# Optimization experiments

Measured on AMD Instinct MI355X. Metric: run time of the kernel, lower is better.

## Reference

```python
import jax, jax.numpy as jnp
import numpy as np

B, S, DIM, H = 2, 2048, 1024, 16
HD = DIM // H  # 64


def setup_inputs() -> dict:
    key = jax.random.key(0)
    ks = jax.random.split(key, 7)
    sc = 1.0 / np.sqrt(DIM)
    gammas = jnp.asarray(1.0 - 2.0 ** (-5.0 - np.arange(H)), jnp.float32)  # RetNet per-head decay
    return {
        "q": jax.random.normal(ks[0], (B, S, DIM), jnp.float32),
        "k": jax.random.normal(ks[1], (B, S, DIM), jnp.float32),
        "v": jax.random.normal(ks[2], (B, S, DIM), jnp.float32),
        "W_in": jax.random.normal(ks[3], (DIM, DIM), jnp.float32) * sc,
        "b_in": jnp.zeros((DIM,), jnp.float32),
        "W_gate": jax.random.normal(ks[4], (DIM, DIM), jnp.float32) * sc,
        "b_gate": jnp.zeros((DIM,), jnp.float32),
        "W_out": jax.random.normal(ks[5], (DIM, DIM), jnp.float32) * sc,
        "b_out": jnp.zeros((DIM,), jnp.float32),
        "gammas": gammas,
    }


def _mamba(x, W_in, b_in, W_gate, b_gate, W_out, b_out):
    # Gated linear recurrence: h_t = a_t * h_{t-1} + u_t  (selective-scan style)
    u = x @ W_in + b_in          # [B,S,D]
    a = jax.nn.sigmoid(x @ W_gate + b_gate)  # [B,S,D] data-dependent decay gate

    def combine(c1, c2):
        a1, u1 = c1
        a2, u2 = c2
        return (a1 * a2, a2 * u1 + u2)

    _, h = jax.lax.associative_scan(combine, (a, u), axis=1)  # parallel scan over S
    return h @ W_out + b_out  # residual=False, dropout=0.0


def _retention(q, k, v, gammas):
    # Per-head decay-masked attention: out = ((Q K^T / sqrt(hd)) * D) V,
    # D[h,n,m] = gamma_h^(n-m) for n>=m else 0 (causal decay kernel).
    def split(x):
        return x.reshape(B, S, H, HD).transpose(0, 2, 1, 3)  # [B,H,S,HD]

    qh, kh, vh = split(q), split(k), split(v)
    idx = jnp.arange(S)
    diff = idx[:, None] - idx[None, :]                        # [S,S]
    expnt = jnp.maximum(diff, 0).astype(jnp.float32)
    D = jnp.where(diff >= 0, gammas[:, None, None] ** expnt, 0.0)  # [H,S,S]
    scores = jnp.einsum("bhnd,bhmd->bhnm", qh, kh) / np.sqrt(HD)
    out = jnp.einsum("bhnm,bhmd->bhnd", scores * D[None], vh)
    return out.transpose(0, 2, 1, 3).reshape(B, S, DIM)


def reference(q, k, v, W_in, b_in, W_gate, b_gate, W_out, b_out, gammas):
    q_proj = _mamba(q, W_in, b_in, W_gate, b_gate, W_out, b_out)
    return _retention(q_proj, k, v, gammas)
```

## Files before the change

kernel.cpp:

```cpp
#include <hip/hip_runtime.h>
#include <math.h>

#define B_  2
#define S_  2048
#define D_  1024
#define H_  16
#define HD_ 64
#define M_  (B_*S_)

typedef unsigned short ushort_t;
typedef unsigned int   uint_t;
typedef __attribute__((ext_vector_type(8))) short bf16x8;
typedef __attribute__((ext_vector_type(4))) float f32x4;

__device__ __forceinline__ ushort_t f2bf(float f) {
    uint_t u = __builtin_bit_cast(uint_t, f);
    u += 0x7FFFu + ((u >> 16) & 1u);
    return (ushort_t)(u >> 16);
}
__device__ __forceinline__ float bf2f(ushort_t h) {
    uint_t u = (uint_t)h << 16;
    return __builtin_bit_cast(float, u);
}
__device__ __forceinline__ uint_t pkt(float lo, float hi) {
    return __builtin_amdgcn_perm(__builtin_bit_cast(uint_t, hi),
                                 __builtin_bit_cast(uint_t, lo), 0x07060302u);
}
__device__ __forceinline__ void dma16(const ushort_t* g, ushort_t* l) {
    __builtin_amdgcn_global_load_lds(
        (const __attribute__((address_space(1))) uint_t*)g,
        (__attribute__((address_space(3))) uint_t*)l, 16, 0, 0);
}
__device__ __forceinline__ bf16x8 fragr(const ushort_t* base, int row, int chunk) {
    return *(const bf16x8*)&base[row * 64 + (((chunk ^ (row & 7)) << 3))];
}

__global__ __launch_bounds__(256)
void transp_cvt3(const float* __restrict__ W0, const float* __restrict__ W1,
                 const float* __restrict__ W2, ushort_t* __restrict__ T0,
                 ushort_t* __restrict__ T1, ushort_t* __restrict__ T2) {
    __shared__ float T[32][36];
    const float*  W  = (blockIdx.z == 0) ? W0 : (blockIdx.z == 1) ? W1 : W2;
    ushort_t*     WT = (blockIdx.z == 0) ? T0 : (blockIdx.z == 1) ? T1 : T2;
    const int kt = blockIdx.x, nt = blockIdx.y;
    const int t = threadIdx.x;
    const int rr = t >> 3, cc = (t & 7) * 4;
    float4 w4 = *(const float4*)(W + (size_t)(kt * 32 + rr) * D_ + nt * 32 + cc);
    T[rr][cc + 0] = w4.x; T[rr][cc + 1] = w4.y; T[rr][cc + 2] = w4.z; T[rr][cc + 3] = w4.w;
    __syncthreads();
    ushort_t o[4];
    #pragma unroll
    for (int j = 0; j < 4; ++j) o[j] = f2bf(T[cc + j][rr]);
    *(ushort4*)(WT + (size_t)(nt * 32 + rr) * D_ + kt * 32 + cc) =
        make_ushort4(o[0], o[1], o[2], o[3]);
}

__global__ __launch_bounds__(256)
void cvt_bf16(const float* __restrict__ X, ushort_t* __restrict__ Y) {
    const int i = (blockIdx.x * 256 + threadIdx.x) * 4;
    float4 x = *(const float4*)(X + i);
    *(ushort4*)(Y + i) = make_ushort4(f2bf(x.x), f2bf(x.y), f2bf(x.z), f2bf(x.w));
}

__global__ __launch_bounds__(256)
void kv_cvt_g(const float* __restrict__ K, const float* __restrict__ V,
              const float* __restrict__ gammas, ushort_t* __restrict__ Kb,
              ushort_t* __restrict__ VT, float* __restrict__ Gg) {
    __shared__ ushort_t Tv[64 * 72];
    __shared__ ushort_t Tk[64 * 72];
    const int mt = blockIdx.x, h = blockIdx.y, b = blockIdx.z;
    const int m0 = mt * 64;
    const int tid = threadIdx.x;
    const int r = tid >> 2, c0 = (tid & 3) * 16;
    const float lg = log2f(gammas[h]);
    const float gm = exp2f(-(float)r * lg);
    {
        const float* src = K + ((size_t)(b * S_ + m0 + r)) * D_ + h * HD_ + c0;
        ushort_t kb[16];
        #pragma unroll
        for (int j4 = 0; j4 < 4; ++j4) {
            float4 x = *(const float4*)(src + j4 * 4);
            kb[j4 * 4 + 0] = f2bf(x.x); kb[j4 * 4 + 1] = f2bf(x.y);
            kb[j4 * 4 + 2] = f2bf(x.z); kb[j4 * 4 + 3] = f2bf(x.w);
        }
        ushort_t* dst = Kb + ((size_t)(b * S_ + m0 + r)) * D_ + h * HD_ + c0;
        *(uint4*)(dst + 0) = *(const uint4*)&kb[0];
        *(uint4*)(dst + 8) = *(const uint4*)&kb[8];
        #pragma unroll
        for (int j = 0; j < 16; ++j) Tk[(c0 + j) * 72 + r] = kb[j];
    }
    {
        const float* src = V + ((size_t)(b * S_ + m0 + r)) * D_ + h * HD_ + c0;
        #pragma unroll
        for (int j4 = 0; j4 < 4; ++j4) {
            float4 x = *(const float4*)(src + j4 * 4);
            Tv[(c0 + j4 * 4 + 0) * 72 + r] = f2bf(x.x * gm);
            Tv[(c0 + j4 * 4 + 1) * 72 + r] = f2bf(x.y * gm);
            Tv[(c0 + j4 * 4 + 2) * 72 + r] = f2bf(x.z * gm);
            Tv[(c0 + j4 * 4 + 3) * 72 + r] = f2bf(x.w * gm);
        }
    }
    __syncthreads();
    {
        ushort_t* dst = VT + ((size_t)((b * H_ + h) * HD_ + r)) * S_ + m0 + c0;
        *(uint4*)(dst + 0) = *(const uint4*)&Tv[r * 72 + c0 + 0];
        *(uint4*)(dst + 8) = *(const uint4*)&Tv[r * 72 + c0 + 8];
    }
    const int w = tid >> 6, lane = tid & 63, quad = lane >> 4, l15 = lane & 15;
    bf16x8 af0 = *(const bf16x8*)&Tv[(w * 16 + l15) * 72 + quad * 8];
    bf16x8 af1 = *(const bf16x8*)&Tv[(w * 16 + l15) * 72 + 32 + quad * 8];
    float* gout = Gg + ((size_t)((b * H_ + h) * 32 + mt)) * 4096;
    #pragma unroll
    for (int kt2 = 0; kt2 < 4; ++kt2) {
        bf16x8 bf0 = *(const bf16x8*)&Tk[(kt2 * 16 + l15) * 72 + quad * 8];
        bf16x8 bf1 = *(const bf16x8*)&Tk[(kt2 * 16 + l15) * 72 + 32 + quad * 8];
        f32x4 g = {};
        g = __builtin_amdgcn_mfma_f32_16x16x32_bf16(af0, bf0, g, 0, 0, 0);
        g = __builtin_amdgcn_mfma_f32_16x16x32_bf16(af1, bf1, g, 0, 0, 0);
        #pragma unroll
        for (int reg = 0; reg < 4; ++reg)
            gout[(w * 16 + quad * 4 + reg) * 64 + kt2 * 16 + l15] = g[reg];
    }
}

__global__ __launch_bounds__(256)
void gemm_dual_scan(const ushort_t* __restrict__ A, const ushort_t* __restrict__ BTi,
                    const ushort_t* __restrict__ BTg, const float* __restrict__ bi,
                    const float* __restrict__ bg, float* __restrict__ Hloc,
                    ushort_t* __restrict__ Pp, float* __restrict__ cA,
                    float* __restrict__ cU) {
    __shared__ ushort_t smem[32768];
    const int tid = threadIdx.x;
    const int n0 = blockIdx.x * 64, m0 = blockIdx.y * 128;
    const int w = tid >> 6, lane = tid & 63, quad = lane >> 4, l15 = lane & 15;
    const int wr = (w >> 1) * 64, wc = (w & 1) * 32;
    const int l8 = lane & 7, lr8 = lane >> 3;

    f32x4 acc_i[4][2] = {};
    f32x4 acc_g[4][2] = {};

    auto stage = [&](int k0, int bufo) {
        #pragma unroll
        for (int t = 0; t < 4; ++t) {
            const int row = w * 32 + t * 8 + lr8;
            const int gc = ((l8 ^ (row & 7)) << 3);
            dma16(A + (size_t)(m0 + row) * D_ + k0 + gc, &smem[bufo + row * 64 + l8 * 8]);
        }
        #pragma unroll
        for (int t = 0; t < 2; ++t) {
            const int row = w * 16 + t * 8 + lr8;
            const int gc = ((l8 ^ (row & 7)) << 3);
            dma16(BTi + (size_t)(n0 + row) * D_ + k0 + gc, &smem[bufo + 8192 + row * 64 + l8 * 8]);
            dma16(BTg + (size_t)(n0 + row) * D_ + k0 + gc, &smem[bufo + 12288 + row * 64 + l8 * 8]);
        }
    };

    stage(0, 0);
    __syncthreads();
    for (int t = 0; t < 16; ++t) {
        const int bufo = (t & 1) * 16384;
        if (t < 15) stage((t + 1) * 64, 16384 - bufo);
        const ushort_t* As = smem + bufo;
        const ushort_t* Bi = smem + bufo + 8192;
        const ushort_t* Bg = smem + bufo + 12288;
        #pragma unroll
        for (int kk = 0; kk < 2; ++kk) {
            bf16x8 af[4], bfi[2], bfg[2];
            #pragma unroll
            for (int i = 0; i < 4; ++i)
                af[i] = fragr(As, wr + 16 * i + l15, kk * 4 + quad);
            #pragma unroll
            for (int j = 0; j < 2; ++j) {
                bfi[j] = fragr(Bi, wc + 16 * j + l15, kk * 4 + quad);
                bfg[j] = fragr(Bg, wc + 16 * j + l15, kk * 4 + quad);
            }
            #pragma unroll
            for (int i = 0; i < 4; ++i)
                #pragma unroll
                for (int j = 0; j < 2; ++j) {
                    acc_i[i][j] = __builtin_amdgcn_mfma_f32_16x16x32_bf16(
                        af[i], bfi[j], acc_i[i][j], 0, 0, 0);
                    acc_g[i][j] = __builtin_amdgcn_mfma_f32_16x16x32_bf16(
                        af[i], bfg[j], acc_g[i][j], 0, 0, 0);
                }
        }
        __syncthreads();
    }

    ushort_t* Us = smem;
    ushort_t* Gu = smem + 8448;
    #pragma unroll
    for (int j = 0; j < 2; ++j) {
        const int n = wc + 16 * j + l15;
        const float bbi = bi[n0 + n], bbg = bg[n0 + n];
        #pragma unroll
        for (int i = 0; i < 4; ++i) {
            #pragma unroll
            for (int r = 0; r < 4; ++r) {
                const int m = wr + 16 * i + quad * 4 + r;
                Us[m * 66 + n] = f2bf(acc_i[i][j][r] + bbi);
                float g = 1.0f / (1.0f + __expf(-(acc_g[i][j][r] + bbg)));
                Gu[m * 66 + n] = (ushort_t)__float2uint_rn(g * 65535.0f);
            }
        }
    }
    __syncthreads();

    const int nl = tid & 63, c = tid >> 6;
    const int gmb = m0 + c * 32;
    const size_t gbase = (size_t)gmb * D_ + n0 + nl;
    float Aa = 1.0f, hh = 0.0f;
    #pragma unroll 4
    for (int j = 0; j < 32; ++j) {
        const float g = (float)Gu[(c * 32 + j) * 66 + nl] * (1.0f / 65535.0f);
        const float u = bf2f(Us[(c * 32 + j) * 66 + nl]);
        Aa *= g;
        hh = fmaf(g, hh, u);
        Pp[gbase + (size_t)j * D_] = f2bf(Aa);
        Hloc[gbase + (size_t)j * D_] = hh;
    }
    const int bb = gmb >> 11;
    const int ch = (gmb & 2047) >> 5;
    const int ci = ((bb * 64 + ch) << 10) + n0 + nl;
    cA[ci] = Aa;
    cU[ci] = hh;
}

__global__ __launch_bounds__(256)
void mid_scan(const float* __restrict__ Gg, const float* __restrict__ gammas,
              ushort_t* __restrict__ Sb, const float* __restrict__ cA,
              const float* __restrict__ cU, float* __restrict__ cIn) {
    const int bi = blockIdx.x;
    if (bi < 128) {
        const int sl = bi & 3, h = (bi >> 2) & 15, b = bi >> 6;
        const float g64 = exp2f(64.0f * log2f(gammas[h]));
        const int r = threadIdx.x >> 4;
        const int cb = (threadIdx.x & 15) * 4;
        const size_t base = ((size_t)((b * H_ + h) * 32)) * 4096 + (sl * 16 + r) * 64 + cb;
        float4 S = make_float4(0.f, 0.f, 0.f, 0.f);
        for (int c = 0; c < 32; ++c) {
            ushort4 sb;
            sb.x = f2bf(S.x); sb.y = f2bf(S.y); sb.z = f2bf(S.z); sb.w = f2bf(S.w);
            *(ushort4*)(Sb + base + (size_t)c * 4096) = sb;
            float4 G = *(const float4*)(Gg + base + (size_t)c * 4096);
            S.x = g64 * (S.x + G.x); S.y = g64 * (S.y + G.y);
            S.z = g64 * (S.z + G.z); S.w = g64 * (S.w + G.w);
        }
        return;
    }
    const int t = (bi - 128) * 256 + threadIdx.x;
    const int d = t & 1023, b = t >> 10;
    float h = 0.0f;
    for (int c0 = 0; c0 < 64; c0 += 16) {
        float Av[16], Uv[16];
        #pragma unroll
        for (int j = 0; j < 16; ++j) {
            const int idx = ((b * 64 + c0 + j) << 10) + d;
            Av[j] = cA[idx]; Uv[j] = cU[idx];
        }
        #pragma unroll
        for (int j = 0; j < 16; ++j) {
            cIn[((b * 64 + c0 + j) << 10) + d] = h;
            h = fmaf(Av[j], h, Uv[j]);
        }
    }
}

__global__ __launch_bounds__(256)
void scan_fix(const float* __restrict__ Hloc, const ushort_t* __restrict__ Pp,
              const float* __restrict__ cIn, ushort_t* __restrict__ hout) {
    const int i = (blockIdx.x * 256 + threadIdx.x) * 4;
    const int m = i >> 10, d = i & 1023;
    const int b = m >> 11, ch = (m & 2047) >> 5;
    float4 hl = *(const float4*)(Hloc + i);
    ushort4 p4 = *(const ushort4*)(Pp + i);
    float4 ci = *(const float4*)(cIn + ((b * 64 + ch) << 10) + d);
    ushort4 o;
    o.x = f2bf(fmaf(ci.x, bf2f(p4.x), hl.x));
    o.y = f2bf(fmaf(ci.y, bf2f(p4.y), hl.y));
    o.z = f2bf(fmaf(ci.z, bf2f(p4.z), hl.z));
    o.w = f2bf(fmaf(ci.w, bf2f(p4.w), hl.w));
    *(ushort4*)(hout + i) = o;
}

__global__ __launch_bounds__(256)
void gemm_out_a(const ushort_t* __restrict__ A, const ushort_t* __restrict__ BT,
                const float* __restrict__ bias, float scale,
                ushort_t* __restrict__ Cb) {
    __shared__ ushort_t smem[24576];
    const int tid = threadIdx.x;
    const int n0 = blockIdx.x * 64, m0 = blockIdx.y * 128;
    const int w = tid >> 6, lane = tid & 63, quad = lane >> 4, l15 = lane & 15;
    const int wr = (w >> 1) * 64, wc = (w & 1) * 32;
    const int l8 = lane & 7, lr8 = lane >> 3;

    f32x4 acc[4][2] = {};

    auto stage = [&](int k0, int bufo) {
        #pragma unroll
        for (int t = 0; t < 4; ++t) {
            const int row = w * 32 + t * 8 + lr8;
            const int gc = ((l8 ^ (row & 7)) << 3);
            dma16(A + (size_t)(m0 + row) * D_ + k0 + gc, &smem[bufo + row * 64 + l8 * 8]);
        }
        #pragma unroll
        for (int t = 0; t < 2; ++t) {
            const int row = w * 16 + t * 8 + lr8;
            const int gc = ((l8 ^ (row & 7)) << 3);
            dma16(BT + (size_t)(n0 + row) * D_ + k0 + gc, &smem[bufo + 8192 + row * 64 + l8 * 8]);
        }
    };

    stage(0, 0);
    __syncthreads();
    for (int t = 0; t < 16; ++t) {
        const int bufo = (t & 1) * 12288;
        if (t < 15) stage((t + 1) * 64, 12288 - bufo);
        const ushort_t* As = smem + bufo;
        const ushort_t* Bs = smem + bufo + 8192;
        #pragma unroll
        for (int kk = 0; kk < 2; ++kk) {
            bf16x8 af[4], bf[2];
            #pragma unroll
            for (int i = 0; i < 4; ++i)
                af[i] = fragr(As, wr + 16 * i + l15, kk * 4 + quad);
            #pragma unroll
            for (int j = 0; j < 2; ++j)
                bf[j] = fragr(Bs, wc + 16 * j + l15, kk * 4 + quad);
            #pragma unroll
            for (int i = 0; i < 4; ++i)
                #pragma unroll
                for (int j = 0; j < 2; ++j)
                    acc[i][j] = __builtin_amdgcn_mfma_f32_16x16x32_bf16(
                        af[i], bf[j], acc[i][j], 0, 0, 0);
        }
        __syncthreads();
    }

    #pragma unroll
    for (int j = 0; j < 2; ++j) {
        const int n = n0 + wc + 16 * j + l15;
        const float bb = bias[n];
        #pragma unroll
        for (int i = 0; i < 4; ++i)
            #pragma unroll
            for (int r = 0; r < 4; ++r) {
                const int m = m0 + wr + 16 * i + quad * 4 + r;
                Cb[(size_t)m * D_ + n] = f2bf((acc[i][j][r] + bb) * scale);
            }
    }
}

__global__ __launch_bounds__(256)
void retention_chunk(const ushort_t* __restrict__ Qb, const ushort_t* __restrict__ Kb,
                     const ushort_t* __restrict__ VT, const ushort_t* __restrict__ Sb,
                     const float* __restrict__ gammas, float* __restrict__ Out) {
    __shared__ ushort_t smem[20480];
    ushort_t* Qs = smem;
    ushort_t* Ks = smem + 4096;
    ushort_t* Vt = smem + 8192;
    ushort_t* Ss = smem + 12288;
    ushort_t* Ps = smem + 16384;
    const int tid = threadIdx.x;
    const int nt = blockIdx.x, h = blockIdx.y, b = blockIdx.z;
    const int n0 = nt * 64;
    const float lg = log2f(gammas[h]);
    const int w = tid >> 6, lane = tid & 63, quad = lane >> 4, l15 = lane & 15;
    const int l8 = lane & 7, lr8 = lane >> 3;
    const int nl = w * 16 + l15;
    const size_t bS = (size_t)b * S_;
    const size_t vrow0 = (size_t)((b * H_ + h) * HD_);
    const size_t sbase = ((size_t)((b * H_ + h) * 32 + nt)) * 4096;

    #pragma unroll
    for (int t = 0; t < 2; ++t) {
        const int row = w * 16 + t * 8 + lr8;
        const int gc = ((l8 ^ (row & 7)) << 3);
        dma16(Qb + (bS + n0 + row) * D_ + h * HD_ + gc, &Qs[row * 64 + l8 * 8]);
        dma16(Kb + (bS + n0 + row) * D_ + h * HD_ + gc, &Ks[row * 64 + l8 * 8]);
        dma16(VT + (vrow0 + row) * S_ + n0 + gc, &Vt[row * 64 + l8 * 8]);
        dma16(Sb + sbase + (size_t)row * 64 + gc, &Ss[row * 64 + l8 * 8]);
    }
    __syncthreads();

    bf16x8 qf0 = fragr(Qs, nl, quad);
    bf16x8 qf1 = fragr(Qs, nl, 4 + quad);

    f32x4 o[4] = {};
    #pragma unroll
    for (int ct = 0; ct < 4; ++ct) {
        bf16x8 sf0 = fragr(Ss, ct * 16 + l15, quad);
        bf16x8 sf1 = fragr(Ss, ct * 16 + l15, 4 + quad);
        o[ct] = __builtin_amdgcn_mfma_f32_16x16x32_bf16(sf0, qf0, o[ct], 0, 0, 0);
        o[ct] = __builtin_amdgcn_mfma_f32_16x16x32_bf16(sf1, qf1, o[ct], 0, 0, 0);
    }
    #pragma unroll
    for (int mt2 = 0; mt2 < 4; ++mt2) {
        bf16x8 kf0 = fragr(Ks, mt2 * 16 + l15, quad);
        bf16x8 kf1 = fragr(Ks, mt2 * 16 + l15, 4 + quad);
        f32x4 s = {};
        s = __builtin_amdgcn_mfma_f32_16x16x32_bf16(kf0, qf0, s, 0, 0, 0);
        s = __builtin_amdgcn_mfma_f32_16x16x32_bf16(kf1, qf1, s, 0, 0, 0);
        const int mbase = mt2 * 16 + quad * 4;
        #pragma unroll
        for (int r = 0; r < 4; ++r)
            if (nl < mbase + r) s[r] = 0.0f;
        uint2 pw; pw.x = pkt(s[0], s[1]); pw.y = pkt(s[2], s[3]);
        const int chunk = mbase >> 3;
        *(uint2*)&Ps[nl * 64 + ((chunk ^ (nl & 7)) << 3) + (mbase & 7)] = pw;
    }
    bf16x8 pf0 = fragr(Ps, nl, quad);
    bf16x8 pf1 = fragr(Ps, nl, 4 + quad);
    #pragma unroll
    for (int ct = 0; ct < 4; ++ct) {
        bf16x8 vf0 = fragr(Vt, ct * 16 + l15, quad);
        bf16x8 vf1 = fragr(Vt, ct * 16 + l15, 4 + quad);
        o[ct] = __builtin_amdgcn_mfma_f32_16x16x32_bf16(vf0, pf0, o[ct], 0, 0, 0);
        o[ct] = __builtin_amdgcn_mfma_f32_16x16x32_bf16(vf1, pf1, o[ct], 0, 0, 0);
    }

    const float esc = exp2f((float)nl * lg);
    const size_t ob = (bS + n0 + nl) * D_ + h * HD_;
    #pragma unroll
    for (int ct = 0; ct < 4; ++ct) {
        f32x4 t = o[ct] * esc;
        *(f32x4*)(Out + ob + ct * 16 + quad * 4) = t;
    }
}

extern "C" void kernel_launch(void* const* d_in, const int* in_sizes, int n_in,
                              void* d_out, int out_size, void* d_ws, size_t ws_size,
                              hipStream_t stream) {
    const float* q      = (const float*)d_in[0];
    const float* k      = (const float*)d_in[1];
    const float* v      = (const float*)d_in[2];
    const float* W_in   = (const float*)d_in[3];
    const float* b_in   = (const float*)d_in[4];
    const float* W_gate = (const float*)d_in[5];
    const float* b_gate = (const float*)d_in[6];
    const float* W_out  = (const float*)d_in[7];
    const float* b_out  = (const float*)d_in[8];
    const float* gammas = (const float*)d_in[9];
    float* out = (float*)d_out;

    char* ws = (char*)d_ws;
    const size_t MB = 1024 * 1024;
    float*    Hloc    = (float*)(ws);
    ushort_t* Pp      = (ushort_t*)(ws + 16 * MB);
    ushort_t* h_bf    = (ushort_t*)(ws + 24 * MB);
    ushort_t* q_bf    = (ushort_t*)(ws + 32 * MB);
    ushort_t* WT_in   = (ushort_t*)(ws + 40 * MB);
    ushort_t* WT_gate = (ushort_t*)(ws + 42 * MB);
    ushort_t* WT_out  = (ushort_t*)(ws + 44 * MB);
    float*    cA      = (float*)(ws + 46 * MB);
    float*    cU      = (float*)(ws + 46 * MB + 512 * 1024);
    float*    cIn     = (float*)(ws + 47 * MB);
    ushort_t* k_bf    = (ushort_t*)(ws + 48 * MB);
    ushort_t* VT      = (ushort_t*)(ws + 56 * MB);
    float*    Gg      = (float*)(ws + 64 * MB);
    ushort_t* Sb      = (ushort_t*)(ws + 80 * MB);
    ushort_t* qp_bf   = q_bf;

    transp_cvt3<<<dim3(D_ / 32, D_ / 32, 3), 256, 0, stream>>>(
        W_in, W_gate, W_out, WT_in, WT_gate, WT_out);
    cvt_bf16<<<(M_ * D_) / (256 * 4), 256, 0, stream>>>(q, q_bf);

    gemm_dual_scan<<<dim3(D_ / 64, M_ / 128), 256, 0, stream>>>(
        q_bf, WT_in, WT_gate, b_in, b_gate, Hloc, Pp, cA, cU);

    kv_cvt_g<<<dim3(S_ / 64, H_, B_), 256, 0, stream>>>(k, v, gammas, k_bf, VT, Gg);

    mid_scan<<<136, 256, 0, stream>>>(Gg, gammas, Sb, cA, cU, cIn);
    scan_fix<<<(M_ * D_) / 1024, 256, 0, stream>>>(Hloc, Pp, cIn, h_bf);

    gemm_out_a<<<dim3(D_ / 64, M_ / 128), 256, 0, stream>>>(
        h_bf, WT_out, b_out, 0.125f, qp_bf);

    retention_chunk<<<dim3(S_ / 64, H_, B_), 256, 0, stream>>>(
        qp_bf, k_bf, VT, Sb, gammas, out);
}
```

Before: 186.1 us.

## Use 4-stage K=32 LDS pipeline with vmcnt waits in projection GEMMs

Both the dual-projection GEMM and the output GEMM move from a double-buffered K=64 tile loop to a four-buffer ring of K=32 tiles, keeping two tiles in flight ahead of compute. Per-iteration syncthreads are replaced by explicit s_waitcnt vmcnt counts plus s_barrier, and MFMA sections run at raised wave priority. The LDS swizzle changes to suit 32-wide rows. This aims to hide global-to-LDS latency better, at the cost of twice as many barriers and hand-tuned wait counts that must exactly match the number of outstanding DMA loads.

Result: slower. 192.4 us (+3.4%).

```diff
diff --git a/kernel.cpp b/kernel.cpp
--- a/kernel.cpp
+++ b/kernel.cpp
@@ -33,6 +33,9 @@
 }
 __device__ __forceinline__ bf16x8 fragr(const ushort_t* base, int row, int chunk) {
     return *(const bf16x8*)&base[row * 64 + (((chunk ^ (row & 7)) << 3))];
+}
+__device__ __forceinline__ bf16x8 fragr32(const ushort_t* base, int row, int chunk) {
+    return *(const bf16x8*)&base[row * 32 + (((chunk ^ ((row >> 1) & 3)) << 3))];
 }
 
 __global__ __launch_bounds__(256)
@@ -134,57 +137,58 @@
     const int n0 = blockIdx.x * 64, m0 = blockIdx.y * 128;
     const int w = tid >> 6, lane = tid & 63, quad = lane >> 4, l15 = lane & 15;
     const int wr = (w >> 1) * 64, wc = (w & 1) * 32;
-    const int l8 = lane & 7, lr8 = lane >> 3;
+    const int l4 = lane & 3, lr4 = lane >> 2;
 
     f32x4 acc_i[4][2] = {};
     f32x4 acc_g[4][2] = {};
 
     auto stage = [&](int k0, int bufo) {
         #pragma unroll
-        for (int t = 0; t < 4; ++t) {
-            const int row = w * 32 + t * 8 + lr8;
-            const int gc = ((l8 ^ (row & 7)) << 3);
-            dma16(A + (size_t)(m0 + row) * D_ + k0 + gc, &smem[bufo + row * 64 + l8 * 8]);
-        }
-        #pragma unroll
         for (int t = 0; t < 2; ++t) {
-            const int row = w * 16 + t * 8 + lr8;
-            const int gc = ((l8 ^ (row & 7)) << 3);
-            dma16(BTi + (size_t)(n0 + row) * D_ + k0 + gc, &smem[bufo + 8192 + row * 64 + l8 * 8]);
-            dma16(BTg + (size_t)(n0 + row) * D_ + k0 + gc, &smem[bufo + 12288 + row * 64 + l8 * 8]);
+            const int row = w * 32 + t * 16 + lr4;
+            const int gc = ((l4 ^ ((row >> 1) & 3)) << 3);
+            dma16(A + (size_t)(m0 + row) * D_ + k0 + gc, &smem[bufo + row * 32 + l4 * 8]);
+        }
+        {
+            const int row = w * 16 + lr4;
+            const int gc = ((l4 ^ ((row >> 1) & 3)) << 3);
+            dma16(BTi + (size_t)(n0 + row) * D_ + k0 + gc, &smem[bufo + 4096 + row * 32 + l4 * 8]);
+            dma16(BTg + (size_t)(n0 + row) * D_ + k0 + gc, &smem[bufo + 6144 + row * 32 + l4 * 8]);
         }
     };
 
     stage(0, 0);
-    __syncthreads();
-    for (int t = 0; t < 16; ++t) {
-        const int bufo = (t & 1) * 16384;
-        if (t < 15) stage((t + 1) * 64, 16384 - bufo);
-        const ushort_t* As = smem + bufo;
-        const ushort_t* Bi = smem + bufo + 8192;
-        const ushort_t* Bg = smem + bufo + 12288;
-        #pragma unroll
-        for (int kk = 0; kk < 2; ++kk) {
-            bf16x8 af[4], bfi[2], bfg[2];
-            #pragma unroll
-            for (int i = 0; i < 4; ++i)
-                af[i] = fragr(As, wr + 16 * i + l15, kk * 4 + quad);
+    stage(32, 8192);
+    stage(64, 16384);
+    for (int t = 0; t < 32; ++t) {
+        if (t < 30)       asm volatile("s_waitcnt vmcnt(8)" ::: "memory");
+        else if (t == 30) asm volatile("s_waitcnt vmcnt(4)" ::: "memory");
+        else              asm volatile("s_waitcnt vmcnt(0)" ::: "memory");
+        __builtin_amdgcn_s_barrier();
+        if (t < 29) stage((t + 3) * 32, ((t + 3) & 3) * 8192);
+        const ushort_t* As = smem + (t & 3) * 8192;
+        const ushort_t* Bi_ = As + 4096;
+        const ushort_t* Bg_ = As + 6144;
+        bf16x8 af[4], bfi[2], bfg[2];
+        #pragma unroll
+        for (int i = 0; i < 4; ++i)
+            af[i] = fragr32(As, wr + 16 * i + l15, quad);
+        #pragma unroll
+        for (int j = 0; j < 2; ++j) {
+            bfi[j] = fragr32(Bi_, wc + 16 * j + l15, quad);
+            bfg[j] = fragr32(Bg_, wc + 16 * j + l15, quad);
+        }
+        __builtin_amdgcn_s_setprio(1);
+        #pragma unroll
+        for (int i = 0; i < 4; ++i)
             #pragma unroll
             for (int j = 0; j < 2; ++j) {
-                bfi[j] = fragr(Bi, wc + 16 * j + l15, kk * 4 + quad);
-                bfg[j] = fragr(Bg, wc + 16 * j + l15, kk * 4 + quad);
+                acc_i[i][j] = __builtin_amdgcn_mfma_f32_16x16x32_bf16(
+                    af[i], bfi[j], acc_i[i][j], 0, 0, 0);
+                acc_g[i][j] = __builtin_amdgcn_mfma_f32_16x16x32_bf16(
+                    af[i], bfg[j], acc_g[i][j], 0, 0, 0);
             }
-            #pragma unroll
-            for (int i = 0; i < 4; ++i)
-                #pragma unroll
-                for (int j = 0; j < 2; ++j) {
-                    acc_i[i][j] = __builtin_amdgcn_mfma_f32_16x16x32_bf16(
-                        af[i], bfi[j], acc_i[i][j], 0, 0, 0);
-                    acc_g[i][j] = __builtin_amdgcn_mfma_f32_16x16x32_bf16(
-                        af[i], bfg[j], acc_g[i][j], 0, 0, 0);
-                }
-        }
-        __syncthreads();
+        __builtin_amdgcn_s_setprio(0);
     }
 
     ushort_t* Us = smem;
@@ -292,49 +296,50 @@
     const int n0 = blockIdx.x * 64, m0 = blockIdx.y * 128;
     const int w = tid >> 6, lane = tid & 63, quad = lane >> 4, l15 = lane & 15;
     const int wr = (w >> 1) * 64, wc = (w & 1) * 32;
-    const int l8 = lane & 7, lr8 = lane >> 3;
+    const int l4 = lane & 3, lr4 = lane >> 2;
 
     f32x4 acc[4][2] = {};
 
     auto stage = [&](int k0, int bufo) {
         #pragma unroll
-        for (int t = 0; t < 4; ++t) {
-            const int row = w * 32 + t * 8 + lr8;
-            const int gc = ((l8 ^ (row & 7)) << 3);
-            dma16(A + (size_t)(m0 + row) * D_ + k0 + gc, &smem[bufo + row * 64 + l8 * 8]);
-        }
-        #pragma unroll
         for (int t = 0; t < 2; ++t) {
-            const int row = w * 16 + t * 8 + lr8;
-            const int gc = ((l8 ^ (row & 7)) << 3);
-            dma16(BT + (size_t)(n0 + row) * D_ + k0 + gc, &smem[bufo + 8192 + row * 64 + l8 * 8]);
+            const int row = w * 32 + t * 16 + lr4;
+            const int gc = ((l4 ^ ((row >> 1) & 3)) << 3);
+            dma16(A + (size_t)(m0 + row) * D_ + k0 + gc, &smem[bufo + row * 32 + l4 * 8]);
+        }
+        {
+            const int row = w * 16 + lr4;
+            const int gc = ((l4 ^ ((row >> 1) & 3)) << 3);
+            dma16(BT + (size_t)(n0 + row) * D_ + k0 + gc, &smem[bufo + 4096 + row * 32 + l4 * 8]);
         }
     };
 
     stage(0, 0);
-    __syncthreads();
-    for (int t = 0; t < 16; ++t) {
-        const int bufo = (t & 1) * 12288;
-        if (t < 15) stage((t + 1) * 64, 12288 - bufo);
-        const ushort_t* As = smem + bufo;
-        const ushort_t* Bs = smem + bufo + 8192;
-        #pragma unroll
-        for (int kk = 0; kk < 2; ++kk) {
-            bf16x8 af[4], bf[2];
-            #pragma unroll
-            for (int i = 0; i < 4; ++i)
-                af[i] = fragr(As, wr + 16 * i + l15, kk * 4 + quad);
+    stage(32, 6144);
+    stage(64, 12288);
+    for (int t = 0; t < 32; ++t) {
+        if (t < 30)       asm volatile("s_waitcnt vmcnt(6)" ::: "memory");
+        else if (t == 30) asm volatile("s_waitcnt vmcnt(3)" ::: "memory");
+        else              asm volatile("s_waitcnt vmcnt(0)" ::: "memory");
+        __builtin_amdgcn_s_barrier();
+        if (t < 29) stage((t + 3) * 32, ((t + 3) & 3) * 6144);
+        const ushort_t* As = smem + (t & 3) * 6144;
+        const ushort_t* Bs = As + 4096;
+        bf16x8 af[4], bf[2];
+        #pragma unroll
+        for (int i = 0; i < 4; ++i)
+            af[i] = fragr32(As, wr + 16 * i + l15, quad);
+        #pragma unroll
+        for (int j = 0; j < 2; ++j)
+            bf[j] = fragr32(Bs, wc + 16 * j + l15, quad);
+        __builtin_amdgcn_s_setprio(1);
+        #pragma unroll
+        for (int i = 0; i < 4; ++i)
             #pragma unroll
             for (int j = 0; j < 2; ++j)
-                bf[j] = fragr(Bs, wc + 16 * j + l15, kk * 4 + quad);
-            #pragma unroll
-            for (int i = 0; i < 4; ++i)
-                #pragma unroll
-                for (int j = 0; j < 2; ++j)
-                    acc[i][j] = __builtin_amdgcn_mfma_f32_16x16x32_bf16(
-                        af[i], bf[j], acc[i][j], 0, 0, 0);
-        }
-        __syncthreads();
+                acc[i][j] = __builtin_amdgcn_mfma_f32_16x16x32_bf16(
+                    af[i], bf[j], acc[i][j], 0, 0, 0);
+        __builtin_amdgcn_s_setprio(0);
     }
 
     #pragma unroll
```

## Fuse kernels: merge prep conversions, co-schedule KV prep with GEMM, fuse out-proj with retention

Applied to the files above, without the earlier changes.

Merges the weight transpose and q conversion into one launch, and folds the K/V conversion plus Gram computation into the dual GEMM grid as extra blocks. It also fuses the output projection GEMM with the chunked retention, so the projected Q tile stays in shared memory instead of round-tripping through global memory. This cuts launch count and one intermediate write/read. The cost is a serialized retention phase inside each GEMM block and heterogeneous blocks within one grid.

New measurement: 178.6 us. 4.0% less time.

```diff
diff --git a/kernel.cpp b/kernel.cpp
--- a/kernel.cpp
+++ b/kernel.cpp
@@ -36,13 +36,22 @@
 }
 
 __global__ __launch_bounds__(256)
-void transp_cvt3(const float* __restrict__ W0, const float* __restrict__ W1,
-                 const float* __restrict__ W2, ushort_t* __restrict__ T0,
-                 ushort_t* __restrict__ T1, ushort_t* __restrict__ T2) {
+void prep(const float* __restrict__ W0, const float* __restrict__ W1,
+          const float* __restrict__ W2, ushort_t* __restrict__ T0,
+          ushort_t* __restrict__ T1, ushort_t* __restrict__ T2,
+          const float* __restrict__ X, ushort_t* __restrict__ Y) {
+    const int bx = blockIdx.x;
+    if (bx >= 3072) {
+        const int i = ((bx - 3072) * 256 + threadIdx.x) * 4;
+        float4 x = *(const float4*)(X + i);
+        *(ushort4*)(Y + i) = make_ushort4(f2bf(x.x), f2bf(x.y), f2bf(x.z), f2bf(x.w));
+        return;
+    }
     __shared__ float T[32][36];
-    const float*  W  = (blockIdx.z == 0) ? W0 : (blockIdx.z == 1) ? W1 : W2;
-    ushort_t*     WT = (blockIdx.z == 0) ? T0 : (blockIdx.z == 1) ? T1 : T2;
-    const int kt = blockIdx.x, nt = blockIdx.y;
+    const int z = bx >> 10;
+    const float*  W  = (z == 0) ? W0 : (z == 1) ? W1 : W2;
+    ushort_t*     WT = (z == 0) ? T0 : (z == 1) ? T1 : T2;
+    const int kt = bx & 31, nt = (bx >> 5) & 31;
     const int t = threadIdx.x;
     const int rr = t >> 3, cc = (t & 7) * 4;
     float4 w4 = *(const float4*)(W + (size_t)(kt * 32 + rr) * D_ + nt * 32 + cc);
@@ -56,83 +65,77 @@
 }
 
 __global__ __launch_bounds__(256)
-void cvt_bf16(const float* __restrict__ X, ushort_t* __restrict__ Y) {
-    const int i = (blockIdx.x * 256 + threadIdx.x) * 4;
-    float4 x = *(const float4*)(X + i);
-    *(ushort4*)(Y + i) = make_ushort4(f2bf(x.x), f2bf(x.y), f2bf(x.z), f2bf(x.w));
-}
-
-__global__ __launch_bounds__(256)
-void kv_cvt_g(const float* __restrict__ K, const float* __restrict__ V,
-              const float* __restrict__ gammas, ushort_t* __restrict__ Kb,
-              ushort_t* __restrict__ VT, float* __restrict__ Gg) {
-    __shared__ ushort_t Tv[64 * 72];
-    __shared__ ushort_t Tk[64 * 72];
-    const int mt = blockIdx.x, h = blockIdx.y, b = blockIdx.z;
-    const int m0 = mt * 64;
-    const int tid = threadIdx.x;
-    const int r = tid >> 2, c0 = (tid & 3) * 16;
-    const float lg = log2f(gammas[h]);
-    const float gm = exp2f(-(float)r * lg);
-    {
-        const float* src = K + ((size_t)(b * S_ + m0 + r)) * D_ + h * HD_ + c0;
-        ushort_t kb[16];
-        #pragma unroll
-        for (int j4 = 0; j4 < 4; ++j4) {
-            float4 x = *(const float4*)(src + j4 * 4);
-            kb[j4 * 4 + 0] = f2bf(x.x); kb[j4 * 4 + 1] = f2bf(x.y);
-            kb[j4 * 4 + 2] = f2bf(x.z); kb[j4 * 4 + 3] = f2bf(x.w);
-        }
-        ushort_t* dst = Kb + ((size_t)(b * S_ + m0 + r)) * D_ + h * HD_ + c0;
-        *(uint4*)(dst + 0) = *(const uint4*)&kb[0];
-        *(uint4*)(dst + 8) = *(const uint4*)&kb[8];
-        #pragma unroll
-        for (int j = 0; j < 16; ++j) Tk[(c0 + j) * 72 + r] = kb[j];
-    }
-    {
-        const float* src = V + ((size_t)(b * S_ + m0 + r)) * D_ + h * HD_ + c0;
-        #pragma unroll
-        for (int j4 = 0; j4 < 4; ++j4) {
-            float4 x = *(const float4*)(src + j4 * 4);
-            Tv[(c0 + j4 * 4 + 0) * 72 + r] = f2bf(x.x * gm);
-            Tv[(c0 + j4 * 4 + 1) * 72 + r] = f2bf(x.y * gm);
-            Tv[(c0 + j4 * 4 + 2) * 72 + r] = f2bf(x.z * gm);
-            Tv[(c0 + j4 * 4 + 3) * 72 + r] = f2bf(x.w * gm);
-        }
-    }
-    __syncthreads();
-    {
-        ushort_t* dst = VT + ((size_t)((b * H_ + h) * HD_ + r)) * S_ + m0 + c0;
-        *(uint4*)(dst + 0) = *(const uint4*)&Tv[r * 72 + c0 + 0];
-        *(uint4*)(dst + 8) = *(const uint4*)&Tv[r * 72 + c0 + 8];
-    }
-    const int w = tid >> 6, lane = tid & 63, quad = lane >> 4, l15 = lane & 15;
-    bf16x8 af0 = *(const bf16x8*)&Tv[(w * 16 + l15) * 72 + quad * 8];
-    bf16x8 af1 = *(const bf16x8*)&Tv[(w * 16 + l15) * 72 + 32 + quad * 8];
-    float* gout = Gg + ((size_t)((b * H_ + h) * 32 + mt)) * 4096;
-    #pragma unroll
-    for (int kt2 = 0; kt2 < 4; ++kt2) {
-        bf16x8 bf0 = *(const bf16x8*)&Tk[(kt2 * 16 + l15) * 72 + quad * 8];
-        bf16x8 bf1 = *(const bf16x8*)&Tk[(kt2 * 16 + l15) * 72 + 32 + quad * 8];
-        f32x4 g = {};
-        g = __builtin_amdgcn_mfma_f32_16x16x32_bf16(af0, bf0, g, 0, 0, 0);
-        g = __builtin_amdgcn_mfma_f32_16x16x32_bf16(af1, bf1, g, 0, 0, 0);
-        #pragma unroll
-        for (int reg = 0; reg < 4; ++reg)
-            gout[(w * 16 + quad * 4 + reg) * 64 + kt2 * 16 + l15] = g[reg];
-    }
-}
-
-__global__ __launch_bounds__(256)
-void gemm_dual_scan(const ushort_t* __restrict__ A, const ushort_t* __restrict__ BTi,
-                    const ushort_t* __restrict__ BTg, const float* __restrict__ bi,
-                    const float* __restrict__ bg, float* __restrict__ Hloc,
-                    ushort_t* __restrict__ Pp, float* __restrict__ cA,
-                    float* __restrict__ cU) {
+void gemm_dual_kv(const ushort_t* __restrict__ A, const ushort_t* __restrict__ BTi,
+                  const ushort_t* __restrict__ BTg, const float* __restrict__ bi,
+                  const float* __restrict__ bg, float* __restrict__ Hloc,
+                  ushort_t* __restrict__ Pp, float* __restrict__ cA,
+                  float* __restrict__ cU,
+                  const float* __restrict__ K, const float* __restrict__ V,
+                  const float* __restrict__ gammas, ushort_t* __restrict__ Kb,
+                  ushort_t* __restrict__ VT, float* __restrict__ Gg) {
     __shared__ ushort_t smem[32768];
     const int tid = threadIdx.x;
-    const int n0 = blockIdx.x * 64, m0 = blockIdx.y * 128;
     const int w = tid >> 6, lane = tid & 63, quad = lane >> 4, l15 = lane & 15;
+
+    if (blockIdx.x >= 512) {
+        ushort_t* Tv = smem;
+        ushort_t* Tk = smem + 64 * 72;
+        const int idx = blockIdx.x - 512;
+        const int mt = idx & 31, h = (idx >> 5) & 15, b = idx >> 9;
+        const int m0 = mt * 64;
+        const int r = tid >> 2, c0 = (tid & 3) * 16;
+        const float lg = log2f(gammas[h]);
+        const float gm = exp2f(-(float)r * lg);
+        {
+            const float* src = K + ((size_t)(b * S_ + m0 + r)) * D_ + h * HD_ + c0;
+            ushort_t kb[16];
+            #pragma unroll
+            for (int j4 = 0; j4 < 4; ++j4) {
+                float4 x = *(const float4*)(src + j4 * 4);
+                kb[j4 * 4 + 0] = f2bf(x.x); kb[j4 * 4 + 1] = f2bf(x.y);
+                kb[j4 * 4 + 2] = f2bf(x.z); kb[j4 * 4 + 3] = f2bf(x.w);
+            }
+            ushort_t* dst = Kb + ((size_t)(b * S_ + m0 + r)) * D_ + h * HD_ + c0;
+            *(uint4*)(dst + 0) = *(const uint4*)&kb[0];
+            *(uint4*)(dst + 8) = *(const uint4*)&kb[8];
+            #pragma unroll
+            for (int j = 0; j < 16; ++j) Tk[(c0 + j) * 72 + r] = kb[j];
+        }
+        {
+            const float* src = V + ((size_t)(b * S_ + m0 + r)) * D_ + h * HD_ + c0;
+            #pragma unroll
+            for (int j4 = 0; j4 < 4; ++j4) {
+                float4 x = *(const float4*)(src + j4 * 4);
+                Tv[(c0 + j4 * 4 + 0) * 72 + r] = f2bf(x.x * gm);
+                Tv[(c0 + j4 * 4 + 1) * 72 + r] = f2bf(x.y * gm);
+                Tv[(c0 + j4 * 4 + 2) * 72 + r] = f2bf(x.z * gm);
+                Tv[(c0 + j4 * 4 + 3) * 72 + r] = f2bf(x.w * gm);
+            }
+        }
+        __syncthreads();
+        {
+            ushort_t* dst = VT + ((size_t)((b * H_ + h) * HD_ + r)) * S_ + m0 + c0;
+            *(uint4*)(dst + 0) = *(const uint4*)&Tv[r * 72 + c0 + 0];
+            *(uint4*)(dst + 8) = *(const uint4*)&Tv[r * 72 + c0 + 8];
+        }
+        bf16x8 af0 = *(const bf16x8*)&Tv[(w * 16 + l15) * 72 + quad * 8];
+        bf16x8 af1 = *(const bf16x8*)&Tv[(w * 16 + l15) * 72 + 32 + quad * 8];
+        float* gout = Gg + ((size_t)((b * H_ + h) * 32 + mt)) * 4096;
+        #pragma unroll
+        for (int kt2 = 0; kt2 < 4; ++kt2) {
+            bf16x8 bf0 = *(const bf16x8*)&Tk[(kt2 * 16 + l15) * 72 + quad * 8];
+            bf16x8 bf1 = *(const bf16x8*)&Tk[(kt2 * 16 + l15) * 72 + 32 + quad * 8];
+            f32x4 g = {};
+            g = __builtin_amdgcn_mfma_f32_16x16x32_bf16(af0, bf0, g, 0, 0, 0);
+            g = __builtin_amdgcn_mfma_f32_16x16x32_bf16(af1, bf1, g, 0, 0, 0);
+            #pragma unroll
+            for (int reg = 0; reg < 4; ++reg)
+                gout[(w * 16 + quad * 4 + reg) * 64 + kt2 * 16 + l15] = g[reg];
+        }
+        return;
+    }
+
+    const int n0 = (blockIdx.x & 15) * 64, m0 = (blockIdx.x >> 4) * 128;
     const int wr = (w >> 1) * 64, wc = (w & 1) * 32;
     const int l8 = lane & 7, lr8 = lane >> 3;
 
@@ -284,12 +287,14 @@
 }
 
 __global__ __launch_bounds__(256)
-void gemm_out_a(const ushort_t* __restrict__ A, const ushort_t* __restrict__ BT,
-                const float* __restrict__ bias, float scale,
-                ushort_t* __restrict__ Cb) {
+void gemm_out_ret(const ushort_t* __restrict__ A, const ushort_t* __restrict__ BT,
+                  const float* __restrict__ bias, const ushort_t* __restrict__ Kb,
+                  const ushort_t* __restrict__ VT, const ushort_t* __restrict__ Sb,
+                  const float* __restrict__ gammas, float* __restrict__ Out) {
     __shared__ ushort_t smem[24576];
     const int tid = threadIdx.x;
-    const int n0 = blockIdx.x * 64, m0 = blockIdx.y * 128;
+    const int h = blockIdx.x;
+    const int n0 = h * 64, m0 = blockIdx.y * 128;
     const int w = tid >> 6, lane = tid & 63, quad = lane >> 4, l15 = lane & 15;
     const int wr = (w >> 1) * 64, wc = (w & 1) * 32;
     const int l8 = lane & 7, lr8 = lane >> 3;
@@ -337,94 +342,93 @@
         __syncthreads();
     }
 
+    ushort_t* Qs = smem;
+    ushort_t* Ks = smem + 8192;
+    ushort_t* Vt = smem + 12288;
+    ushort_t* Ss = smem + 16384;
+    ushort_t* Ps = smem + 20480;
     #pragma unroll
     for (int j = 0; j < 2; ++j) {
-        const int n = n0 + wc + 16 * j + l15;
-        const float bb = bias[n];
+        const int n = wc + 16 * j + l15;
+        const float bb = bias[n0 + n];
         #pragma unroll
         for (int i = 0; i < 4; ++i)
             #pragma unroll
             for (int r = 0; r < 4; ++r) {
-                const int m = m0 + wr + 16 * i + quad * 4 + r;
-                Cb[(size_t)m * D_ + n] = f2bf((acc[i][j][r] + bb) * scale);
+                const int m = wr + 16 * i + quad * 4 + r;
+                Qs[m * 64 + (((n >> 3) ^ (m & 7)) << 3) + (n & 7)] =
+                    f2bf((acc[i][j][r] + bb) * 0.125f);
             }
     }
-}
-
-__global__ __launch_bounds__(256)
-void retention_chunk(const ushort_t* __restrict__ Qb, const ushort_t* __restrict__ Kb,
-                     const ushort_t* __restrict__ VT, const ushort_t* __restrict__ Sb,
-                     const float* __restrict__ gammas, float* __restrict__ Out) {
-    __shared__ ushort_t smem[20480];
-    ushort_t* Qs = smem;
-    ushort_t* Ks = smem + 4096;
-    ushort_t* Vt = smem + 8192;
-    ushort_t* Ss = smem + 12288;
-    ushort_t* Ps = smem + 16384;
-    const int tid = threadIdx.x;
-    const int nt = blockIdx.x, h = blockIdx.y, b = blockIdx.z;
-    const int n0 = nt * 64;
+    __syncthreads();
+
     const float lg = log2f(gammas[h]);
-    const int w = tid >> 6, lane = tid & 63, quad = lane >> 4, l15 = lane & 15;
-    const int l8 = lane & 7, lr8 = lane >> 3;
     const int nl = w * 16 + l15;
-    const size_t bS = (size_t)b * S_;
-    const size_t vrow0 = (size_t)((b * H_ + h) * HD_);
-    const size_t sbase = ((size_t)((b * H_ + h) * 32 + nt)) * 4096;
-
-    #pragma unroll
-    for (int t = 0; t < 2; ++t) {
-        const int row = w * 16 + t * 8 + lr8;
-        const int gc = ((l8 ^ (row & 7)) << 3);
-        dma16(Qb + (bS + n0 + row) * D_ + h * HD_ + gc, &Qs[row * 64 + l8 * 8]);
-        dma16(Kb + (bS + n0 + row) * D_ + h * HD_ + gc, &Ks[row * 64 + l8 * 8]);
-        dma16(VT + (vrow0 + row) * S_ + n0 + gc, &Vt[row * 64 + l8 * 8]);
-        dma16(Sb + sbase + (size_t)row * 64 + gc, &Ss[row * 64 + l8 * 8]);
-    }
-    __syncthreads();
-
-    bf16x8 qf0 = fragr(Qs, nl, quad);
-    bf16x8 qf1 = fragr(Qs, nl, 4 + quad);
-
-    f32x4 o[4] = {};
-    #pragma unroll
-    for (int ct = 0; ct < 4; ++ct) {
-        bf16x8 sf0 = fragr(Ss, ct * 16 + l15, quad);
-        bf16x8 sf1 = fragr(Ss, ct * 16 + l15, 4 + quad);
-        o[ct] = __builtin_amdgcn_mfma_f32_16x16x32_bf16(sf0, qf0, o[ct], 0, 0, 0);
-        o[ct] = __builtin_amdgcn_mfma_f32_16x16x32_bf16(sf1, qf1, o[ct], 0, 0, 0);
-    }
-    #pragma unroll
-    for (int mt2 = 0; mt2 < 4; ++mt2) {
-        bf16x8 kf0 = fragr(Ks, mt2 * 16 + l15, quad);
-        bf16x8 kf1 = fragr(Ks, mt2 * 16 + l15, 4 + quad);
-        f32x4 s = {};
-        s = __builtin_amdgcn_mfma_f32_16x16x32_bf16(kf0, qf0, s, 0, 0, 0);
-        s = __builtin_amdgcn_mfma_f32_16x16x32_bf16(kf1, qf1, s, 0, 0, 0);
-        const int mbase = mt2 * 16 + quad * 4;
-        #pragma unroll
-        for (int r = 0; r < 4; ++r)
-            if (nl < mbase + r) s[r] = 0.0f;
-        uint2 pw; pw.x = pkt(s[0], s[1]); pw.y = pkt(s[2], s[3]);
-        const int chunk = mbase >> 3;
-        *(uint2*)&Ps[nl * 64 + ((chunk ^ (nl & 7)) << 3) + (mbase & 7)] = pw;
-    }
-    bf16x8 pf0 = fragr(Ps, nl, quad);
-    bf16x8 pf1 = fragr(Ps, nl, 4 + quad);
-    #pragma unroll
-    for (int ct = 0; ct < 4; ++ct) {
-        bf16x8 vf0 = fragr(Vt, ct * 16 + l15, quad);
-        bf16x8 vf1 = fragr(Vt, ct * 16 + l15, 4 + quad);
-        o[ct] = __builtin_amdgcn_mfma_f32_16x16x32_bf16(vf0, pf0, o[ct], 0, 0, 0);
-        o[ct] = __builtin_amdgcn_mfma_f32_16x16x32_bf16(vf1, pf1, o[ct], 0, 0, 0);
-    }
-
-    const float esc = exp2f((float)nl * lg);
-    const size_t ob = (bS + n0 + nl) * D_ + h * HD_;
-    #pragma unroll
-    for (int ct = 0; ct < 4; ++ct) {
-        f32x4 t = o[ct] * esc;
-        *(f32x4*)(Out + ob + ct * 16 + quad * 4) = t;
+
+    for (int sc = 0; sc < 2; ++sc) {
+        const int mrow = m0 + sc * 64;
+        const int bb2 = mrow >> 11;
+        const int s0 = mrow & 2047;
+        const int nt2 = s0 >> 6;
+        const size_t bS = (size_t)bb2 * S_;
+        const size_t vrow0 = (size_t)((bb2 * H_ + h) * HD_);
+        const size_t sbase = ((size_t)((bb2 * H_ + h) * 32 + nt2)) * 4096;
+        const ushort_t* Qsub = Qs + sc * 64 * 64;
+
+        #pragma unroll
+        for (int t = 0; t < 2; ++t) {
+            const int row = w * 16 + t * 8 + lr8;
+            const int gc = ((l8 ^ (row & 7)) << 3);
+            dma16(Kb + (bS + s0 + row) * D_ + h * HD_ + gc, &Ks[row * 64 + l8 * 8]);
+            dma16(VT + (vrow0 + row) * S_ + s0 + gc, &Vt[row * 64 + l8 * 8]);
+            dma16(Sb + sbase + (size_t)row * 64 + gc, &Ss[row * 64 + l8 * 8]);
+        }
+        __syncthreads();
+
+        bf16x8 qf0 = fragr(Qsub, nl, quad);
+        bf16x8 qf1 = fragr(Qsub, nl, 4 + quad);
+
+        f32x4 o[4] = {};
+        #pragma unroll
+        for (int ct = 0; ct < 4; ++ct) {
+            bf16x8 sf0 = fragr(Ss, ct * 16 + l15, quad);
+            bf16x8 sf1 = fragr(Ss, ct * 16 + l15, 4 + quad);
+            o[ct] = __builtin_amdgcn_mfma_f32_16x16x32_bf16(sf0, qf0, o[ct], 0, 0, 0);
+            o[ct] = __builtin_amdgcn_mfma_f32_16x16x32_bf16(sf1, qf1, o[ct], 0, 0, 0);
+        }
+        #pragma unroll
+        for (int mt2 = 0; mt2 < 4; ++mt2) {
+            bf16x8 kf0 = fragr(Ks, mt2 * 16 + l15, quad);
+            bf16x8 kf1 = fragr(Ks, mt2 * 16 + l15, 4 + quad);
+            f32x4 s = {};
+            s = __builtin_amdgcn_mfma_f32_16x16x32_bf16(kf0, qf0, s, 0, 0, 0);
+            s = __builtin_amdgcn_mfma_f32_16x16x32_bf16(kf1, qf1, s, 0, 0, 0);
+            const int mbase = mt2 * 16 + quad * 4;
+            #pragma unroll
+            for (int r = 0; r < 4; ++r)
+                if (nl < mbase + r) s[r] = 0.0f;
+            uint2 pw; pw.x = pkt(s[0], s[1]); pw.y = pkt(s[2], s[3]);
+            const int chunk = mbase >> 3;
+            *(uint2*)&Ps[nl * 64 + ((chunk ^ (nl & 7)) << 3) + (mbase & 7)] = pw;
+        }
+        bf16x8 pf0 = fragr(Ps, nl, quad);
+        bf16x8 pf1 = fragr(Ps, nl, 4 + quad);
+        #pragma unroll
+        for (int ct = 0; ct < 4; ++ct) {
+            bf16x8 vf0 = fragr(Vt, ct * 16 + l15, quad);
+            bf16x8 vf1 = fragr(Vt, ct * 16 + l15, 4 + quad);
+            o[ct] = __builtin_amdgcn_mfma_f32_16x16x32_bf16(vf0, pf0, o[ct], 0, 0, 0);
+            o[ct] = __builtin_amdgcn_mfma_f32_16x16x32_bf16(vf1, pf1, o[ct], 0, 0, 0);
+        }
+
+        const float esc = exp2f((float)nl * lg);
+        const size_t ob = (bS + s0 + nl) * D_ + h * HD_;
+        #pragma unroll
+        for (int ct = 0; ct < 4; ++ct) {
+            f32x4 t = o[ct] * esc;
+            *(f32x4*)(Out + ob + ct * 16 + quad * 4) = t;
+        }
+        __syncthreads();
     }
 }
 
@@ -459,23 +463,17 @@
     ushort_t* VT      = (ushort_t*)(ws + 56 * MB);
     float*    Gg      = (float*)(ws + 64 * MB);
     ushort_t* Sb      = (ushort_t*)(ws + 80 * MB);
-    ushort_t* qp_bf   = q_bf;
-
-    transp_cvt3<<<dim3(D_ / 32, D_ / 32, 3), 256, 0, stream>>>(
-        W_in, W_gate, W_out, WT_in, WT_gate, WT_out);
-    cvt_bf16<<<(M_ * D_) / (256 * 4), 256, 0, stream>>>(q, q_bf);
-
-    gemm_dual_scan<<<dim3(D_ / 64, M_ / 128), 256, 0, stream>>>(
-        q_bf, WT_in, WT_gate, b_in, b_gate, Hloc, Pp, cA, cU);
-
-    kv_cvt_g<<<dim3(S_ / 64, H_, B_), 256, 0, stream>>>(k, v, gammas, k_bf, VT, Gg);
+
+    prep<<<3072 + (M_ * D_) / (256 * 4), 256, 0, stream>>>(
+        W_in, W_gate, W_out, WT_in, WT_gate, WT_out, q, q_bf);
+
+    gemm_dual_kv<<<512 + 1024, 256, 0, stream>>>(
+        q_bf, WT_in, WT_gate, b_in, b_gate, Hloc, Pp, cA, cU,
+        k, v, gammas, k_bf, VT, Gg);
 
     mid_scan<<<136, 256, 0, stream>>>(Gg, gammas, Sb, cA, cU, cIn);
     scan_fix<<<(M_ * D_) / 1024, 256, 0, stream>>>(Hloc, Pp, cIn, h_bf);
 
-    gemm_out_a<<<dim3(D_ / 64, M_ / 128), 256, 0, stream>>>(
-        h_bf, WT_out, b_out, 0.125f, qp_bf);
-
-    retention_chunk<<<dim3(S_ / 64, H_, B_), 256, 0, stream>>>(
-        qp_bf, k_bf, VT, Sb, gammas, out);
-}
+    gemm_out_ret<<<dim3(H_, M_ / 128), 256, 0, stream>>>(
+        h_bf, WT_out, b_out, k_bf, VT, Sb, gammas, out);
+}
```
